# Kernel optimization log

Hardware: AMD Instinct MI355X
Metric: run time of the kernel (lower is better)

The kernel has to match this reference:

```python
import jax, jax.numpy as jnp
import numpy as np

DIM = 256
HEADS = 8
W0, W1 = 8, 8
N = W0 * W1
SCALE = (DIM // HEADS) ** (-0.5)


def _rel_pos_index(w0, w1):
    ch = np.arange(w0)
    cw = np.arange(w1)
    coords = np.stack(np.meshgrid(ch, cw, indexing='ij')).reshape(2, -1)  # (2, N)
    rel = coords[:, :, None] - coords[:, None, :]                          # (2, N, N)
    rel = rel.transpose(1, 2, 0).copy()                                    # (N, N, 2)
    rel[:, :, 0] += w0 - 1
    rel[:, :, 1] += w1 - 1
    rel[:, :, 0] *= 2 * w1 - 1
    return rel.sum(-1)                                                     # (N, N)

REL_IDX = jnp.asarray(_rel_pos_index(W0, W1))


def setup_inputs() -> dict:
    key = jax.random.key(0)
    ks = jax.random.split(key, 9)
    B, C, H, W = 8, DIM, 128, 128
    s = DIM ** -0.5
    return {
        'x': jax.random.normal(ks[0], (B, C, H, W), jnp.float32),
        'embedding': jax.random.normal(ks[1], (1, N, DIM), jnp.float32),
        'rpb_table': jax.random.normal(ks[2], ((2 * W0 - 1) * (2 * W1 - 1), HEADS), jnp.float32),
        'q_w': jax.random.normal(ks[3], (DIM, DIM), jnp.float32) * s,
        'q_b': jnp.zeros((DIM,), jnp.float32),
        'kv_w': jax.random.normal(ks[4], (2 * DIM, DIM), jnp.float32) * s,
        'kv_b': jnp.zeros((2 * DIM,), jnp.float32),
        'proj_w': jax.random.normal(ks[5], (DIM, DIM), jnp.float32) * s,
        'proj_b': jnp.zeros((DIM,), jnp.float32),
    }


def reference(x, embedding, rpb_table, q_w, q_b, kv_w, kv_b, proj_w, proj_b):
    B, C, H, W = x.shape
    # window_partition (faithful to the original, incl. its discarded-permute view):
    # torch views the contiguous (B,C,H,W) buffer as (B, H//w0, w0, W//w1, w1, C)
    win = x.reshape(B, H // W0, W0, W // W1, W1, C)
    win = win.transpose(0, 1, 3, 2, 4, 5).reshape(-1, N, C)  # (Bw, N, C)
    Bw = win.shape[0]
    hd = C // HEADS

    q = jnp.einsum('bnc,dc->bnd', jnp.broadcast_to(embedding, (Bw, N, C)), q_w) + q_b
    q = q.reshape(Bw, N, HEADS, hd).transpose(0, 2, 1, 3)      # (Bw, h, N, hd)
    kv = jnp.einsum('bnc,dc->bnd', win, kv_w) + kv_b           # (Bw, N, 2C)
    kv = kv.reshape(Bw, N, 2, HEADS, hd).transpose(2, 0, 3, 1, 4)
    k, v = kv[0], kv[1]                                         # (Bw, h, N, hd)

    bias = rpb_table[REL_IDX.reshape(-1)].reshape(N, N, HEADS).transpose(2, 0, 1)  # (h, N, N)

    attn = jnp.einsum('bhnd,bhmd->bhnm', q * SCALE, k) + bias[None]
    attn = jax.nn.softmax(attn, axis=-1)
    out = jnp.einsum('bhnm,bhmd->bhnd', attn, v)
    out = out.transpose(0, 2, 1, 3).reshape(Bw, N, C)
    out = jnp.einsum('bnc,dc->bnd', out, proj_w) + proj_b
    return out
```

## Files before the change

### kernel.cpp

```cpp
#include <hip/hip_runtime.h>

typedef short bf16x8 __attribute__((ext_vector_type(8)));
typedef float f32x4 __attribute__((ext_vector_type(4)));
typedef unsigned u32;
typedef unsigned short u16;
typedef unsigned u32x4v __attribute__((ext_vector_type(4)));
typedef unsigned u32x2v __attribute__((ext_vector_type(2)));

union UV { u32x4v u; bf16x8 v; };

__device__ __forceinline__ u16 f2bf(float f){
  u32 u = __float_as_uint(f);
  u += 0x7FFFu + ((u>>16)&1u);
  return (u16)(u>>16);
}
__device__ __forceinline__ u32 pack2(float lo, float hi){
  return (u32)f2bf(lo) | ((u32)f2bf(hi)<<16);
}

__global__ void k_qs(const float* __restrict__ emb, const float* __restrict__ q_w,
                     const float* __restrict__ q_b, u16* __restrict__ q_s){
  const int n = blockIdx.x;
  const int d = threadIdx.x;
  const float4* er = (const float4*)(emb + n*256);
  const float4* wr = (const float4*)(q_w + d*256);
  float acc = 0.f;
  for(int c=0;c<64;++c){
    float4 e = er[c], w = wr[c];
    acc += e.x*w.x + e.y*w.y + e.z*w.z + e.w*w.w;
  }
  acc += q_b[d];
  q_s[n*256 + d] = f2bf(acc * 0.17677669529663687f);
}

__global__ void k_bias(const float* __restrict__ rpb, float* __restrict__ bias){
  const int o = blockIdx.x*256 + threadIdx.x;
  const int h = o>>12, n = (o>>6)&63, m = o&63;
  const int idx = ((n>>3)-(m>>3)+7)*15 + ((n&7)-(m&7)+7);
  bias[o] = rpb[idx*8 + h];
}

__global__ void k_wcvt(const float* __restrict__ kv_w, const float* __restrict__ proj_w,
                       u32* __restrict__ kvb, u32* __restrict__ pjb){
  const int i = blockIdx.x*256 + threadIdx.x;
  if(i < 65536) kvb[i] = pack2(kv_w[2*i], kv_w[2*i+1]);
  else { int j = i - 65536; pjb[j] = pack2(proj_w[2*j], proj_w[2*j+1]); }
}

__global__ __launch_bounds__(256,2) void k_fused(const float* __restrict__ x, const u16* __restrict__ kvw,
                                                 const float* __restrict__ kv_b, const u16* __restrict__ q_s,
                                                 const float* __restrict__ bias, const u16* __restrict__ pjw,
                                                 const float* __restrict__ proj_b, float* __restrict__ out){
  __shared__ char smem[69632];
  char* regA = smem;
  char* regB = smem + 36864;

  const int bw = blockIdx.x;
  const int b = bw>>8, h1 = (bw>>4)&15, w1 = bw&15;
  const int base = b*4194304 + h1*262144 + w1*2048;
  const int tid = threadIdx.x;
  const int w = tid>>6, l = tid&63, g = l>>4, li = l&15;

  {
    #pragma unroll
    for(int i=0;i<8;++i){
      int p = i*256 + tid;
      int n = p>>5;
      int c4 = (2*p)&63;
      const float4* gp = (const float4*)(x + base + (n>>3)*32768 + (n&7)*256 + c4*4);
      float4 lo = gp[0], hi = gp[1];
      u32x4v d = { pack2(lo.x,lo.y), pack2(lo.z,lo.w), pack2(hi.x,hi.y), pack2(hi.z,hi.w) };
      *(u32x4v*)(regA + ((p*16) ^ ((n&7)<<4))) = d;
    }
  }
  __syncthreads();

  {
    f32x4 acc[4][8];
    #pragma unroll
    for(int ct=0;ct<8;++ct){
      float bv = kv_b[w*128 + ct*16 + li];
      #pragma unroll
      for(int rt=0;rt<4;++rt) acc[rt][ct] = (f32x4){bv,bv,bv,bv};
    }
    for(int ks=0;ks<8;++ks){
      bf16x8 a[4];
      #pragma unroll
      for(int rt=0;rt<4;++rt){
        int n = rt*16 + li;
        a[rt] = *(const bf16x8*)(regA + ((n*512 + ks*64 + g*16) ^ ((n&7)<<4)));
      }
      #pragma unroll
      for(int ct=0;ct<8;++ct){
        bf16x8 bfr = *(const bf16x8*)(kvw + (w*128 + ct*16 + li)*256 + ks*32 + g*8);
        #pragma unroll
        for(int rt=0;rt<4;++rt)
          acc[rt][ct] = __builtin_amdgcn_mfma_f32_16x16x32_bf16(a[rt], bfr, acc[rt][ct], 0,0,0);
      }
    }
    __syncthreads();

    if(w < 2){
      #pragma unroll
      for(int ct=0;ct<8;++ct){
        int col = w*128 + ct*16 + li;
        #pragma unroll
        for(int rt=0;rt<4;++rt)
          #pragma unroll
          for(int r=0;r<4;++r){
            int row = rt*16 + 4*g + r;
            *(u16*)(regA + ((row*512 + col*2) ^ ((row&7)<<4))) = f2bf(acc[rt][ct][r]);
          }
      }
    } else {
      #pragma unroll
      for(int ct=0;ct<8;++ct){
        int c2 = (w-2)*128 + ct*16 + li;
        int hv = c2>>5, e = c2&31;
        #pragma unroll
        for(int rt=0;rt<4;++rt){
          u32x2v d;
          d[0] = pack2(acc[rt][ct][0], acc[rt][ct][1]);
          d[1] = pack2(acc[rt][ct][2], acc[rt][ct][3]);
          int m0 = rt*16 + 4*g;
          *(u32x2v*)(regB + (((hv*32 + e)*128 + m0*2) ^ ((e&7)<<4))) = d;
        }
      }
    }
  }
  __syncthreads();

  bf16x8 qf[2][4], kf[2][4];
  #pragma unroll
  for(int hh=0;hh<2;++hh){
    const int h = w + 4*hh;
    #pragma unroll
    for(int rt=0;rt<4;++rt) qf[hh][rt] = *(const bf16x8*)(q_s + (rt*16+li)*256 + h*32 + g*8);
    #pragma unroll
    for(int ct=0;ct<4;++ct){
      int row = ct*16 + li;
      kf[hh][ct] = *(const bf16x8*)(regA + ((row*512 + (h*32+g*8)*2) ^ ((row&7)<<4)));
    }
  }
  __syncthreads();

  u32* pb = (u32*)regA + w*2304;
  const int odd = l & 1;

  #pragma unroll
  for(int hh=0;hh<2;++hh){
    const int h = w + 4*hh;
    f32x4 S[4][4];
    #pragma unroll
    for(int rt=0;rt<4;++rt){
      #pragma unroll
      for(int ct=0;ct<4;++ct){
        const float* bp = bias + h*4096 + (rt*16 + 4*g)*64 + ct*16 + li;
        f32x4 c = { bp[0], bp[64], bp[128], bp[192] };
        S[rt][ct] = __builtin_amdgcn_mfma_f32_16x16x32_bf16(qf[hh][rt], kf[hh][ct], c, 0,0,0);
      }
    }
    float rs[4][4];
    #pragma unroll
    for(int rt=0;rt<4;++rt){
      #pragma unroll
      for(int r=0;r<4;++r){
        float m_ = fmaxf(fmaxf(S[rt][0][r],S[rt][1][r]), fmaxf(S[rt][2][r],S[rt][3][r]));
        m_ = fmaxf(m_, __shfl_xor(m_,1));
        m_ = fmaxf(m_, __shfl_xor(m_,2));
        m_ = fmaxf(m_, __shfl_xor(m_,4));
        m_ = fmaxf(m_, __shfl_xor(m_,8));
        float e0 = __expf(S[rt][0][r]-m_), e1 = __expf(S[rt][1][r]-m_);
        float e2 = __expf(S[rt][2][r]-m_), e3 = __expf(S[rt][3][r]-m_);
        S[rt][0][r]=e0; S[rt][1][r]=e1; S[rt][2][r]=e2; S[rt][3][r]=e3;
        float s_ = e0+e1+e2+e3;
        s_ += __shfl_xor(s_,1); s_ += __shfl_xor(s_,2); s_ += __shfl_xor(s_,4); s_ += __shfl_xor(s_,8);
        rs[rt][r] = 1.0f/s_;
      }
    }
    #pragma unroll
    for(int rt=0;rt<4;++rt){
      #pragma unroll
      for(int ct=0;ct<4;++ct){
        float v0=S[rt][ct][0], v1=S[rt][ct][1], v2=S[rt][ct][2], v3=S[rt][ct][3];
        float o0=__shfl_xor(v0,1), o1=__shfl_xor(v1,1), o2=__shfl_xor(v2,1), o3=__shfl_xor(v3,1);
        u32 d0 = odd ? pack2(o2,v2) : pack2(v0,o0);
        u32 d1 = odd ? pack2(o3,v3) : pack2(v1,o1);
        int r0 = odd ? 2 : 0;
        int cp = ct*8 + (li>>1);
        pb[(rt*16 + 4*g + r0    )*36 + cp] = d0;
        pb[(rt*16 + 4*g + r0 + 1)*36 + cp] = d1;
      }
    }
    f32x4 O[4][2];
    #pragma unroll
    for(int rt=0;rt<4;++rt){ O[rt][0]=(f32x4){0,0,0,0}; O[rt][1]=(f32x4){0,0,0,0}; }
    #pragma unroll
    for(int ks=0;ks<2;++ks){
      bf16x8 pf[4];
      #pragma unroll
      for(int rt=0;rt<4;++rt){
        UV t; t.u = *(const u32x4v*)(pb + (rt*16+li)*36 + ks*16 + g*4);
        pf[rt] = t.v;
      }
      #pragma unroll
      for(int c2=0;c2<2;++c2){
        int e = c2*16 + li;
        bf16x8 vf = *(const bf16x8*)(regB + (((h*32 + e)*128 + (ks*32+g*8)*2) ^ ((e&7)<<4)));
        #pragma unroll
        for(int rt=0;rt<4;++rt)
          O[rt][c2] = __builtin_amdgcn_mfma_f32_16x16x32_bf16(pf[rt], vf, O[rt][c2], 0,0,0);
      }
    }
    #pragma unroll
    for(int rt=0;rt<4;++rt)
      #pragma unroll
      for(int c2=0;c2<2;++c2)
        #pragma unroll
        for(int r=0;r<4;++r){
          int row = rt*16 + 4*g + r;
          *(u16*)(regB + h*4096 + ((row*64 + (c2*16+li)*2) ^ ((row&7)<<4))) = f2bf(O[rt][c2][r]*rs[rt][r]);
        }
  }
  __syncthreads();

  {
    f32x4 acc[4][4];
    #pragma unroll
    for(int ct=0;ct<4;++ct){
      float bv = proj_b[w*64 + ct*16 + li];
      #pragma unroll
      for(int rt=0;rt<4;++rt) acc[rt][ct] = (f32x4){bv,bv,bv,bv};
    }
    for(int ks=0;ks<8;++ks){
      bf16x8 a[4];
      #pragma unroll
      for(int rt=0;rt<4;++rt){
        int row = rt*16 + li;
        a[rt] = *(const bf16x8*)(regB + ks*4096 + ((row*64 + g*16) ^ ((row&7)<<4)));
      }
      #pragma unroll
      for(int ct=0;ct<4;++ct){
        bf16x8 bfr = *(const bf16x8*)(pjw + (w*64 + ct*16 + li)*256 + ks*32 + g*8);
        #pragma unroll
        for(int rt=0;rt<4;++rt)
          acc[rt][ct] = __builtin_amdgcn_mfma_f32_16x16x32_bf16(a[rt], bfr, acc[rt][ct], 0,0,0);
      }
    }
    #pragma unroll
    for(int rt=0;rt<4;++rt)
      #pragma unroll
      for(int ct=0;ct<4;++ct)
        #pragma unroll
        for(int r=0;r<4;++r)
          out[(bw*64 + rt*16 + 4*g + r)*256 + w*64 + ct*16 + li] = acc[rt][ct][r];
  }
}

extern "C" void kernel_launch(void* const* d_in, const int* in_sizes, int n_in,
                              void* d_out, int out_size, void* d_ws, size_t ws_size,
                              hipStream_t stream){
  (void)in_sizes; (void)n_in; (void)out_size;
  const float* x      = (const float*)d_in[0];
  const float* emb    = (const float*)d_in[1];
  const float* rpb    = (const float*)d_in[2];
  const float* q_w    = (const float*)d_in[3];
  const float* q_b    = (const float*)d_in[4];
  const float* kv_w   = (const float*)d_in[5];
  const float* kv_b   = (const float*)d_in[6];
  const float* proj_w = (const float*)d_in[7];
  const float* proj_b = (const float*)d_in[8];
  float* out = (float*)d_out;

  char* ws = (char*)d_ws;
  if(ws_size < (size_t)557056) return;
  u16* q_s   = (u16*)(ws);
  float* bias= (float*)(ws + 32768);
  u32* kvb   = (u32*)(ws + 163840);
  u32* pjb   = (u32*)(ws + 425984);

  k_qs   <<<  64, 256, 0, stream>>>(emb, q_w, q_b, q_s);
  k_bias <<< 128, 256, 0, stream>>>(rpb, bias);
  k_wcvt <<< 384, 256, 0, stream>>>(kv_w, proj_w, kvb, pjb);
  k_fused<<<2048, 256, 0, stream>>>(x, (const u16*)kvb, kv_b, q_s, bias,
                                    (const u16*)pjb, proj_b, out);
}
```

Baseline: 402.5 us.

## Use 8 waves per window, shrink shared memory, switch attention to 32x32 MFMA

The fused window-attention kernel now runs 512 threads per block (one wave per head) instead of 256, and reuses a single 32 KB shared buffer in staged phases where it previously used 68 KB in two regions. The KV projection work is split across 8 waves. QK^T and PV use 32x32x16 MFMA with a transposed S layout, and the P operand is built in registers through cross-half shuffles rather than staged through LDS. The goals are higher occupancy and fewer LDS round trips. The cost is extra barriers to serialise reuse of the single buffer, plus a harmless leftover dead load statement.

```diff
diff --git a/kernel.cpp b/kernel.cpp
--- a/kernel.cpp
+++ b/kernel.cpp
@@ -2,6 +2,7 @@
 
 typedef short bf16x8 __attribute__((ext_vector_type(8)));
 typedef float f32x4 __attribute__((ext_vector_type(4)));
+typedef float f32x16 __attribute__((ext_vector_type(16)));
 typedef unsigned u32;
 typedef unsigned short u16;
 typedef unsigned u32x4v __attribute__((ext_vector_type(4)));
@@ -47,213 +48,225 @@
   else { int j = i - 65536; pjb[j] = pack2(proj_w[2*j], proj_w[2*j+1]); }
 }
 
-__global__ __launch_bounds__(256,2) void k_fused(const float* __restrict__ x, const u16* __restrict__ kvw,
+__global__ __launch_bounds__(512,4) void k_fused(const float* __restrict__ x, const u16* __restrict__ kvw,
                                                  const float* __restrict__ kv_b, const u16* __restrict__ q_s,
                                                  const float* __restrict__ bias, const u16* __restrict__ pjw,
                                                  const float* __restrict__ proj_b, float* __restrict__ out){
-  __shared__ char smem[69632];
-  char* regA = smem;
-  char* regB = smem + 36864;
+  __shared__ char R1[32768];
 
   const int bw = blockIdx.x;
   const int b = bw>>8, h1 = (bw>>4)&15, w1 = bw&15;
   const int base = b*4194304 + h1*262144 + w1*2048;
   const int tid = threadIdx.x;
   const int w = tid>>6, l = tid&63, g = l>>4, li = l&15;
-
-  {
-    #pragma unroll
-    for(int i=0;i<8;++i){
-      int p = i*256 + tid;
-      int n = p>>5;
-      int c4 = (2*p)&63;
-      const float4* gp = (const float4*)(x + base + (n>>3)*32768 + (n&7)*256 + c4*4);
-      float4 lo = gp[0], hi = gp[1];
-      u32x4v d = { pack2(lo.x,lo.y), pack2(lo.z,lo.w), pack2(hi.x,hi.y), pack2(hi.z,hi.w) };
-      *(u32x4v*)(regA + ((p*16) ^ ((n&7)<<4))) = d;
-    }
-  }
-  __syncthreads();
-
-  {
-    f32x4 acc[4][8];
-    #pragma unroll
-    for(int ct=0;ct<8;++ct){
-      float bv = kv_b[w*128 + ct*16 + li];
-      #pragma unroll
-      for(int rt=0;rt<4;++rt) acc[rt][ct] = (f32x4){bv,bv,bv,bv};
-    }
-    for(int ks=0;ks<8;++ks){
-      bf16x8 a[4];
-      #pragma unroll
-      for(int rt=0;rt<4;++rt){
-        int n = rt*16 + li;
-        a[rt] = *(const bf16x8*)(regA + ((n*512 + ks*64 + g*16) ^ ((n&7)<<4)));
-      }
-      #pragma unroll
-      for(int ct=0;ct<8;++ct){
-        bf16x8 bfr = *(const bf16x8*)(kvw + (w*128 + ct*16 + li)*256 + ks*32 + g*8);
-        #pragma unroll
-        for(int rt=0;rt<4;++rt)
-          acc[rt][ct] = __builtin_amdgcn_mfma_f32_16x16x32_bf16(a[rt], bfr, acc[rt][ct], 0,0,0);
-      }
-    }
-    __syncthreads();
-
-    if(w < 2){
-      #pragma unroll
-      for(int ct=0;ct<8;++ct){
-        int col = w*128 + ct*16 + li;
-        #pragma unroll
-        for(int rt=0;rt<4;++rt)
-          #pragma unroll
-          for(int r=0;r<4;++r){
-            int row = rt*16 + 4*g + r;
-            *(u16*)(regA + ((row*512 + col*2) ^ ((row&7)<<4))) = f2bf(acc[rt][ct][r]);
-          }
-      }
-    } else {
-      #pragma unroll
-      for(int ct=0;ct<8;++ct){
-        int c2 = (w-2)*128 + ct*16 + li;
-        int hv = c2>>5, e = c2&31;
-        #pragma unroll
-        for(int rt=0;rt<4;++rt){
-          u32x2v d;
-          d[0] = pack2(acc[rt][ct][0], acc[rt][ct][1]);
-          d[1] = pack2(acc[rt][ct][2], acc[rt][ct][3]);
-          int m0 = rt*16 + 4*g;
-          *(u32x2v*)(regB + (((hv*32 + e)*128 + m0*2) ^ ((e&7)<<4))) = d;
-        }
-      }
-    }
-  }
-  __syncthreads();
-
-  bf16x8 qf[2][4], kf[2][4];
-  #pragma unroll
-  for(int hh=0;hh<2;++hh){
-    const int h = w + 4*hh;
-    #pragma unroll
-    for(int rt=0;rt<4;++rt) qf[hh][rt] = *(const bf16x8*)(q_s + (rt*16+li)*256 + h*32 + g*8);
+  const int l31 = l&31, hi = l>>5;
+
+  #pragma unroll
+  for(int i=0;i<4;++i){
+    int p = i*512 + tid;
+    int n = p>>5;
+    int c4 = (2*p)&63;
+    const float4* gp = (const float4*)(x + base + (n>>3)*32768 + (n&7)*256 + c4*4);
+    float4 lo = gp[0], hh = gp[1];
+    u32x4v d = { pack2(lo.x,lo.y), pack2(lo.z,lo.w), pack2(hh.x,hh.y), pack2(hh.z,hh.w) };
+    *(u32x4v*)(R1 + ((p*16) ^ ((n&7)<<4)));
+    *(u32x4v*)(R1 + ((p*16) ^ ((n&7)<<4))) = d;
+  }
+  __syncthreads();
+
+  f32x4 acc[4][4];
+  #pragma unroll
+  for(int ct=0;ct<4;++ct){
+    float bv = kv_b[w*64 + ct*16 + li];
+    #pragma unroll
+    for(int rt=0;rt<4;++rt) acc[rt][ct] = (f32x4){bv,bv,bv,bv};
+  }
+  for(int ks=0;ks<8;++ks){
+    bf16x8 a[4];
+    #pragma unroll
+    for(int rt=0;rt<4;++rt){
+      int n = rt*16 + li;
+      a[rt] = *(const bf16x8*)(R1 + ((n*512 + ks*64 + g*16) ^ ((n&7)<<4)));
+    }
     #pragma unroll
     for(int ct=0;ct<4;++ct){
-      int row = ct*16 + li;
-      kf[hh][ct] = *(const bf16x8*)(regA + ((row*512 + (h*32+g*8)*2) ^ ((row&7)<<4)));
-    }
-  }
-  __syncthreads();
-
-  u32* pb = (u32*)regA + w*2304;
-  const int odd = l & 1;
-
-  #pragma unroll
-  for(int hh=0;hh<2;++hh){
-    const int h = w + 4*hh;
-    f32x4 S[4][4];
-    #pragma unroll
-    for(int rt=0;rt<4;++rt){
-      #pragma unroll
-      for(int ct=0;ct<4;++ct){
-        const float* bp = bias + h*4096 + (rt*16 + 4*g)*64 + ct*16 + li;
-        f32x4 c = { bp[0], bp[64], bp[128], bp[192] };
-        S[rt][ct] = __builtin_amdgcn_mfma_f32_16x16x32_bf16(qf[hh][rt], kf[hh][ct], c, 0,0,0);
-      }
-    }
-    float rs[4][4];
-    #pragma unroll
-    for(int rt=0;rt<4;++rt){
-      #pragma unroll
-      for(int r=0;r<4;++r){
-        float m_ = fmaxf(fmaxf(S[rt][0][r],S[rt][1][r]), fmaxf(S[rt][2][r],S[rt][3][r]));
-        m_ = fmaxf(m_, __shfl_xor(m_,1));
-        m_ = fmaxf(m_, __shfl_xor(m_,2));
-        m_ = fmaxf(m_, __shfl_xor(m_,4));
-        m_ = fmaxf(m_, __shfl_xor(m_,8));
-        float e0 = __expf(S[rt][0][r]-m_), e1 = __expf(S[rt][1][r]-m_);
-        float e2 = __expf(S[rt][2][r]-m_), e3 = __expf(S[rt][3][r]-m_);
-        S[rt][0][r]=e0; S[rt][1][r]=e1; S[rt][2][r]=e2; S[rt][3][r]=e3;
-        float s_ = e0+e1+e2+e3;
-        s_ += __shfl_xor(s_,1); s_ += __shfl_xor(s_,2); s_ += __shfl_xor(s_,4); s_ += __shfl_xor(s_,8);
-        rs[rt][r] = 1.0f/s_;
-      }
-    }
-    #pragma unroll
-    for(int rt=0;rt<4;++rt){
-      #pragma unroll
-      for(int ct=0;ct<4;++ct){
-        float v0=S[rt][ct][0], v1=S[rt][ct][1], v2=S[rt][ct][2], v3=S[rt][ct][3];
-        float o0=__shfl_xor(v0,1), o1=__shfl_xor(v1,1), o2=__shfl_xor(v2,1), o3=__shfl_xor(v3,1);
-        u32 d0 = odd ? pack2(o2,v2) : pack2(v0,o0);
-        u32 d1 = odd ? pack2(o3,v3) : pack2(v1,o1);
-        int r0 = odd ? 2 : 0;
-        int cp = ct*8 + (li>>1);
-        pb[(rt*16 + 4*g + r0    )*36 + cp] = d0;
-        pb[(rt*16 + 4*g + r0 + 1)*36 + cp] = d1;
-      }
-    }
-    f32x4 O[4][2];
-    #pragma unroll
-    for(int rt=0;rt<4;++rt){ O[rt][0]=(f32x4){0,0,0,0}; O[rt][1]=(f32x4){0,0,0,0}; }
-    #pragma unroll
-    for(int ks=0;ks<2;++ks){
-      bf16x8 pf[4];
-      #pragma unroll
-      for(int rt=0;rt<4;++rt){
-        UV t; t.u = *(const u32x4v*)(pb + (rt*16+li)*36 + ks*16 + g*4);
-        pf[rt] = t.v;
-      }
-      #pragma unroll
-      for(int c2=0;c2<2;++c2){
-        int e = c2*16 + li;
-        bf16x8 vf = *(const bf16x8*)(regB + (((h*32 + e)*128 + (ks*32+g*8)*2) ^ ((e&7)<<4)));
-        #pragma unroll
-        for(int rt=0;rt<4;++rt)
-          O[rt][c2] = __builtin_amdgcn_mfma_f32_16x16x32_bf16(pf[rt], vf, O[rt][c2], 0,0,0);
-      }
-    }
-    #pragma unroll
-    for(int rt=0;rt<4;++rt)
-      #pragma unroll
-      for(int c2=0;c2<2;++c2)
+      bf16x8 bfr = *(const bf16x8*)(kvw + (w*64 + ct*16 + li)*256 + ks*32 + g*8);
+      #pragma unroll
+      for(int rt=0;rt<4;++rt)
+        acc[rt][ct] = __builtin_amdgcn_mfma_f32_16x16x32_bf16(a[rt], bfr, acc[rt][ct], 0,0,0);
+    }
+  }
+  __syncthreads();
+
+  const int h = w;
+  bf16x8 qf[2][2];
+  #pragma unroll
+  for(int nt=0;nt<2;++nt)
+    #pragma unroll
+    for(int ks=0;ks<2;++ks)
+      qf[nt][ks] = *(const bf16x8*)(q_s + (nt*32 + l31)*256 + h*32 + ks*16 + hi*8);
+
+  if(w < 4){
+    #pragma unroll
+    for(int ct=0;ct<4;++ct){
+      int col = w*64 + ct*16 + li;
+      #pragma unroll
+      for(int rt=0;rt<4;++rt)
         #pragma unroll
         for(int r=0;r<4;++r){
           int row = rt*16 + 4*g + r;
-          *(u16*)(regB + h*4096 + ((row*64 + (c2*16+li)*2) ^ ((row&7)<<4))) = f2bf(O[rt][c2][r]*rs[rt][r]);
+          *(u16*)(R1 + ((row*512 + col*2) ^ ((row&7)<<4))) = f2bf(acc[rt][ct][r]);
         }
+    }
+  }
+  __syncthreads();
+
+  bf16x8 kf[2][2];
+  #pragma unroll
+  for(int mt=0;mt<2;++mt)
+    #pragma unroll
+    for(int ks=0;ks<2;++ks){
+      int row = mt*32 + l31;
+      kf[mt][ks] = *(const bf16x8*)(R1 + ((row*512 + (h*32 + ks*16 + hi*8)*2) ^ ((row&7)<<4)));
+    }
+  __syncthreads();
+
+  if(w >= 4){
+    #pragma unroll
+    for(int ct=0;ct<4;++ct){
+      int c2 = (w-4)*64 + ct*16 + li;
+      int hv = c2>>5, e = c2&31;
+      #pragma unroll
+      for(int rt=0;rt<4;++rt){
+        u32x2v d;
+        d[0] = pack2(acc[rt][ct][0], acc[rt][ct][1]);
+        d[1] = pack2(acc[rt][ct][2], acc[rt][ct][3]);
+        int m0 = rt*16 + 4*g;
+        *(u32x2v*)(R1 + (((hv*32 + e)*128 + m0*2) ^ ((e&7)<<4))) = d;
+      }
+    }
+  }
+  __syncthreads();
+
+  f32x16 S[2][2];
+  #pragma unroll
+  for(int mt=0;mt<2;++mt)
+    #pragma unroll
+    for(int nt=0;nt<2;++nt){
+      int n = nt*32 + l31;
+      const float* bp = bias + h*4096 + n*64 + mt*32 + 4*hi;
+      #pragma unroll
+      for(int q=0;q<4;++q){
+        float4 bv = *(const float4*)(bp + q*8);
+        S[mt][nt][4*q+0] = bv.x; S[mt][nt][4*q+1] = bv.y;
+        S[mt][nt][4*q+2] = bv.z; S[mt][nt][4*q+3] = bv.w;
+      }
+    }
+  #pragma unroll
+  for(int ks=0;ks<2;++ks)
+    #pragma unroll
+    for(int mt=0;mt<2;++mt)
+      #pragma unroll
+      for(int nt=0;nt<2;++nt)
+        S[mt][nt] = __builtin_amdgcn_mfma_f32_32x32x16_bf16(kf[mt][ks], qf[nt][ks], S[mt][nt], 0,0,0);
+
+  float rs[2];
+  u32 cb0[2][8], cb1[2][8];
+  #pragma unroll
+  for(int nt=0;nt<2;++nt){
+    float t[16];
+    #pragma unroll
+    for(int j=0;j<16;++j) t[j] = fmaxf(S[0][nt][j], S[1][nt][j]);
+    #pragma unroll
+    for(int s=8;s>0;s>>=1)
+      #pragma unroll
+      for(int j=0;j<8;++j) if(j<s) t[j] = fmaxf(t[j], t[j+s]);
+    float mx = fmaxf(t[0], __shfl_xor(t[0], 32));
+    float sm[16];
+    #pragma unroll
+    for(int j=0;j<16;++j){
+      S[0][nt][j] = __expf(S[0][nt][j] - mx);
+      S[1][nt][j] = __expf(S[1][nt][j] - mx);
+      sm[j] = S[0][nt][j] + S[1][nt][j];
+    }
+    #pragma unroll
+    for(int s=8;s>0;s>>=1)
+      #pragma unroll
+      for(int j=0;j<8;++j) if(j<s) sm[j] += sm[j+s];
+    float total = sm[0] + __shfl_xor(sm[0], 32);
+    rs[nt] = 1.0f/total;
+    #pragma unroll
+    for(int mt=0;mt<2;++mt)
+      #pragma unroll
+      for(int q=0;q<4;++q){
+        cb0[nt][mt*4+q] = pack2(S[mt][nt][4*q+0], S[mt][nt][4*q+1]);
+        cb1[nt][mt*4+q] = pack2(S[mt][nt][4*q+2], S[mt][nt][4*q+3]);
+      }
+  }
+
+  f32x16 O[2];
+  O[0] = (f32x16)(0.f); O[1] = (f32x16)(0.f);
+  #pragma unroll
+  for(int ks2=0;ks2<4;++ks2){
+    bf16x8 vf = *(const bf16x8*)(R1 + (((h*32 + l31)*128 + (ks2*16 + hi*8)*2) ^ ((l31&7)<<4)));
+    #pragma unroll
+    for(int nt=0;nt<2;++nt){
+      u32 A0 = cb0[nt][2*ks2], B0 = cb0[nt][2*ks2+1];
+      u32 A1 = cb1[nt][2*ks2], B1 = cb1[nt][2*ks2+1];
+      u32 r0 = (u32)__shfl_xor((int)(hi ? A0 : B0), 32);
+      u32 r1 = (u32)__shfl_xor((int)(hi ? A1 : B1), 32);
+      u32 w0 = hi ? r0 : A0;
+      u32 w1 = hi ? r1 : A1;
+      u32 w2 = hi ? B0 : r0;
+      u32 w3 = hi ? B1 : r1;
+      UV t; t.u = (u32x4v){w0,w1,w2,w3};
+      O[nt] = __builtin_amdgcn_mfma_f32_32x32x16_bf16(vf, t.v, O[nt], 0,0,0);
+    }
+  }
+
+  #pragma unroll
+  for(int nt=0;nt<2;++nt){
+    int n = nt*32 + l31;
+    #pragma unroll
+    for(int q=0;q<4;++q){
+      u32x2v d;
+      d[0] = pack2(O[nt][4*q+0]*rs[nt], O[nt][4*q+1]*rs[nt]);
+      d[1] = pack2(O[nt][4*q+2]*rs[nt], O[nt][4*q+3]*rs[nt]);
+      *(u32x2v*)(R1 + h*4096 + ((n*64 + (8*q + 4*hi)*2) ^ ((n&7)<<4))) = d;
+    }
   }
   __syncthreads();
 
   {
-    f32x4 acc[4][4];
-    #pragma unroll
-    for(int ct=0;ct<4;++ct){
-      float bv = proj_b[w*64 + ct*16 + li];
-      #pragma unroll
-      for(int rt=0;rt<4;++rt) acc[rt][ct] = (f32x4){bv,bv,bv,bv};
+    f32x4 pacc[4][2];
+    #pragma unroll
+    for(int ct=0;ct<2;++ct){
+      float bv = proj_b[w*32 + ct*16 + li];
+      #pragma unroll
+      for(int rt=0;rt<4;++rt) pacc[rt][ct] = (f32x4){bv,bv,bv,bv};
     }
     for(int ks=0;ks<8;++ks){
       bf16x8 a[4];
       #pragma unroll
       for(int rt=0;rt<4;++rt){
         int row = rt*16 + li;
-        a[rt] = *(const bf16x8*)(regB + ks*4096 + ((row*64 + g*16) ^ ((row&7)<<4)));
-      }
-      #pragma unroll
-      for(int ct=0;ct<4;++ct){
-        bf16x8 bfr = *(const bf16x8*)(pjw + (w*64 + ct*16 + li)*256 + ks*32 + g*8);
+        a[rt] = *(const bf16x8*)(R1 + ks*4096 + ((row*64 + g*16) ^ ((row&7)<<4)));
+      }
+      #pragma unroll
+      for(int ct=0;ct<2;++ct){
+        bf16x8 bfr = *(const bf16x8*)(pjw + (w*32 + ct*16 + li)*256 + ks*32 + g*8);
         #pragma unroll
         for(int rt=0;rt<4;++rt)
-          acc[rt][ct] = __builtin_amdgcn_mfma_f32_16x16x32_bf16(a[rt], bfr, acc[rt][ct], 0,0,0);
+          pacc[rt][ct] = __builtin_amdgcn_mfma_f32_16x16x32_bf16(a[rt], bfr, pacc[rt][ct], 0,0,0);
       }
     }
     #pragma unroll
     for(int rt=0;rt<4;++rt)
       #pragma unroll
-      for(int ct=0;ct<4;++ct)
+      for(int ct=0;ct<2;++ct)
         #pragma unroll
         for(int r=0;r<4;++r)
-          out[(bw*64 + rt*16 + 4*g + r)*256 + w*64 + ct*16 + li] = acc[rt][ct][r];
+          out[(bw*64 + rt*16 + 4*g + r)*256 + w*32 + ct*16 + li] = pacc[rt][ct][r];
   }
 }
 
@@ -282,6 +295,6 @@
   k_qs   <<<  64, 256, 0, stream>>>(emb, q_w, q_b, q_s);
   k_bias <<< 128, 256, 0, stream>>>(rpb, bias);
   k_wcvt <<< 384, 256, 0, stream>>>(kv_w, proj_w, kvb, pjb);
-  k_fused<<<2048, 256, 0, stream>>>(x, (const u16*)kvb, kv_b, q_s, bias,
+  k_fused<<<2048, 512, 0, stream>>>(x, (const u16*)kvb, kv_b, q_s, bias,
                                     (const u16*)pjb, proj_b, out);
 }
```

Result: faster. 364.7 us (-9.4%).
